# Kernel tuning notes

Measured on AMD Instinct MI355X. Metric: run time of the kernel, lower is better.

## Reference

```python
import jax, jax.numpy as jnp
import numpy as np

NINP, NHID, NOUT = 400, 600, 400
HS = NHID + NOUT          # h_size = nhid + nout
NLEVELS, K, AUX_FREQ = 40, 2, 20
DILATION = [1]


def setup_inputs() -> dict:
    key = jax.random.key(0)
    ks = jax.random.split(key, 6)
    B, T = 8, 256
    bound = 0.01  # matches init_weights normal_(0, 0.01)
    return {
        "X": jax.random.normal(ks[0], (B, NINP, T), jnp.float32),
        "hid": jax.random.normal(ks[1], (B, HS, 1), jnp.float32),
        "cell": jax.random.normal(ks[2], (B, HS, 1), jnp.float32),
        "w1": jax.random.normal(ks[3], (4 * HS, NINP, K), jnp.float32) * bound,
        "w2": jax.random.normal(ks[4], (4 * HS, HS, K), jnp.float32) * bound,
        "b2": jax.random.normal(ks[5], (4 * HS,), jnp.float32) * bound,
    }


def _conv1d(x, w, d):
    # x: [B, Cin, T_padded], w: [Cout, Cin, K] -> [B, Cout, T]
    return jax.lax.conv_general_dilated(
        x, w, window_strides=(1,), padding='VALID', rhs_dilation=(d,),
        dimension_numbers=('NCH', 'OIH', 'NCH'))


def _forward(X, hid, cell, w1, w2, b2):
    B, _, T = X.shape
    ht = jnp.zeros((B, HS, T), X.dtype)
    ct = jnp.zeros((B, HS, T), X.dtype)

    # Input-side convolution is weight-tied and X never changes across levels,
    # so (like the torch dict cache) compute it once per distinct dilation.
    conv1 = {}
    for d in set(DILATION):
        pad = (K - 1) * d
        xp = jnp.pad(X, ((0, 0), (0, 0), (pad, 0)))
        conv1[d] = _conv1d(xp, w1, d)

    aux = []
    for i in range(NLEVELS):
        d = DILATION[i % len(DILATION)]
        pad = (K - 1) * d
        # causal left-pad of the hidden stream, filled with the initial hid
        z1 = jnp.concatenate([jnp.broadcast_to(hid, (B, HS, pad)), ht], axis=2)
        out = conv1[d] + _conv1d(z1, w2, d) + b2[None, :, None]  # [B, 4*HS, T]
        # shifted cell state, first d steps filled with the initial cell
        ct_1 = jnp.concatenate(
            [jnp.broadcast_to(cell, (B, HS, d)), ct[:, :, :-d]], axis=2)
        it = jax.nn.sigmoid(out[:, :HS])
        ot = jax.nn.sigmoid(out[:, HS:2 * HS])
        gt = jnp.tanh(out[:, 2 * HS:3 * HS])
        ft = jax.nn.sigmoid(out[:, 3 * HS:])
        ct = ft * ct_1 + it * gt
        ht = ot * jnp.tanh(ct)
        if i % AUX_FREQ == AUX_FREQ - 1:
            aux.append(ht[:, -NOUT:])  # [B, nout, T]

    out_main = jnp.transpose(ht[:, -NOUT:], (0, 2, 1))            # [B, T, nout]
    hc = (ht[:, :, -1:], ct[:, :, -1:])                            # ([B,HS,1], [B,HS,1])
    aux_outs = jnp.transpose(jnp.stack(aux, axis=0), (1, 0, 3, 2))  # [B, n_aux, T, nout]
    return out_main, hc, aux_outs


def reference(X, hid, cell, w1, w2, b2):
    return _forward(X, hid, cell, w1, w2, b2)
```

## Files before the change

kernel.cpp:

```cpp
#include <hip/hip_runtime.h>
#include <hip/hip_bf16.h>
#include <math.h>

typedef __bf16 bf16;
typedef __bf16 bf16x8 __attribute__((ext_vector_type(8)));
typedef __bf16 bf16x4 __attribute__((ext_vector_type(4)));
typedef float f32x4 __attribute__((ext_vector_type(4)));
typedef float f32x16 __attribute__((ext_vector_type(16)));
typedef unsigned int u32;
typedef u32 u32x4 __attribute__((ext_vector_type(4)));

#define NINP 400
#define HS   1000
#define HP   1024
#define B_   8
#define T_   256
#define NT   2048
#define K2   2048
#define K1   1024
#define M_   4096

#define HT_OFF   819200
#define CT_OFF   827200
#define AUX_OFF  835200

__device__ __forceinline__ float sigm(float x) { return 1.0f / (1.0f + expf(-x)); }


__global__ void repack_w1(const float* __restrict__ w1, bf16* __restrict__ W1q) {
  int idx = blockIdx.x * 256 + threadIdx.x;
  if (idx >= M_ * K1) return;
  int m = idx >> 10, k = idx & 1023;
  int g = (m >> 3) & 3, h = (m >> 5) * 8 + (m & 7);
  float v = 0.0f;
  if (h < HS) {
    int c = g * HS + h;
    if (k < 512) { if (k < NINP) v = w1[(size_t)c * (NINP * 2) + k * 2 + 0]; }
    else { int j = k - 512; if (j < NINP) v = w1[(size_t)c * (NINP * 2) + j * 2 + 1]; }
  }
  W1q[idx] = (bf16)v;
}

__global__ void repack_w2(const float* __restrict__ w2, bf16* __restrict__ W2q) {
  int idx = blockIdx.x * 256 + threadIdx.x;
  if (idx >= M_ * K2) return;
  int m = idx >> 11, k = idx & 2047;
  int g = (m >> 3) & 3, h = (m >> 5) * 8 + (m & 7);
  float v = 0.0f;
  if (h < HS) {
    int c = g * HS + h;
    if (k < HP) { if (k < HS) v = w2[(size_t)c * (HS * 2) + k * 2 + 0]; }
    else { int j = k - HP; if (j < HS) v = w2[(size_t)c * (HS * 2) + j * 2 + 1]; }
  }
  W2q[idx] = (bf16)v;
}

__global__ void build_xt(const float* __restrict__ X, bf16* __restrict__ XT) {
  int idx = blockIdx.x * 256 + threadIdx.x;
  if (idx >= NT * K1) return;
  int n = idx >> 10, k = idx & 1023;
  int b = n >> 8, t = n & (T_ - 1);
  float v = 0.0f;
  if (k < 512) { if (k < NINP && t > 0) v = X[((size_t)b * NINP + k) * T_ + t - 1]; }
  else { int j = k - 512; if (j < NINP) v = X[((size_t)b * NINP + j) * T_ + t]; }
  XT[idx] = (bf16)v;
}

__global__ void build_hc(const float* __restrict__ hid, const float* __restrict__ cell,
                         bf16* __restrict__ hidp, float* __restrict__ cellp) {
  int idx = blockIdx.x * 256 + threadIdx.x;
  if (idx >= B_ * HP) return;
  int b = idx >> 10, k = idx & (HP - 1);
  hidp[idx]  = (k < HS) ? (bf16)hid[b * HS + k] : (bf16)0.0f;
  cellp[idx] = (k < HS) ? cell[b * HS + k] : 0.0f;
}


template <bool GATED>
__global__ __launch_bounds__(256, 2) void gemm_step(
    const bf16* __restrict__ A,
    const bf16* __restrict__ Bsrc,
    const bf16* __restrict__ hidp,
    const bf16* __restrict__ CbIn,
    bf16* __restrict__ CbOut,
    const float* __restrict__ b2,
    const bf16* __restrict__ ctprev,
    const float* __restrict__ cellp,
    bf16* __restrict__ ctnew,
    bf16* __restrict__ Hnew,
    int K) {
  __shared__ bf16 As[2][128][64];
  __shared__ bf16 Bs[2][128][64];

  const int tid = threadIdx.x;
  const int lane = tid & 63;
  const int w = tid >> 6;
  const int mh = w >> 1, nh = w & 1;
  const int c8 = tid & 7;
  const int sr = tid >> 3;
  const int row32 = lane & 31;
  const int q2 = lane >> 5;
  const int physw = ((c8 + sr) & 7) * 8;

  int n0, bm;
  if (GATED) {
    const int L = blockIdx.y * gridDim.x + blockIdx.x;
    bm = (L & 7) * 4 + (L >> 7);
    n0 = ((L >> 3) & 15) * 128;
  } else {
    n0 = blockIdx.x * 128;
    bm = blockIdx.y;
  }

  const int NIT = K >> 6;
  const bf16* Abase = A + (size_t)(bm * 128 + sr) * K + c8 * 8;

  auto loadA = [&](int site, int k0) -> u32x4 {
    return *(const u32x4*)(Abase + (size_t)site * 32 * K + k0);
  };
  auto loadB = [&](int site, int k0) -> u32x4 {
    const int n = n0 + site * 32 + sr;
    const bf16* bp;
    if (GATED) {
      if (k0 < HP) {
        const int t = n & (T_ - 1);
        bp = (t == 0) ? (hidp + (size_t)(n >> 8) * HP + k0)
                      : (Bsrc + (size_t)(n - 1) * HP + k0);
      } else {
        bp = Bsrc + (size_t)n * HP + (k0 - HP);
      }
    } else {
      bp = Bsrc + (size_t)n * K + k0;
    }
    return *(const u32x4*)(bp + c8 * 8);
  };

  f32x16 acc[2][2];
#pragma unroll
  for (int i = 0; i < 2; ++i)
#pragma unroll
    for (int j = 0; j < 2; ++j)
#pragma unroll
      for (int e = 0; e < 16; ++e) acc[i][j][e] = 0.0f;

  u32x4 ra[4], rb[4];
#pragma unroll
  for (int s = 0; s < 4; ++s) { ra[s] = loadA(s, 0); rb[s] = loadB(s, 0); }
#pragma unroll
  for (int s = 0; s < 4; ++s) {
    *(u32x4*)&As[0][s * 32 + sr][physw] = ra[s];
    *(u32x4*)&Bs[0][s * 32 + sr][physw] = rb[s];
  }

  for (int it = 0; it < NIT; ++it) {
    const int p = it & 1;
    if (it + 1 < NIT) {
      const int k0 = (it + 1) << 6;
#pragma unroll
      for (int s = 0; s < 4; ++s) { ra[s] = loadA(s, k0); rb[s] = loadB(s, k0); }
    }
    __syncthreads();
#pragma unroll
    for (int kc = 0; kc < 4; ++kc) {
      const int l = kc * 2 + q2;
      bf16x8 av[2], bv[2];
#pragma unroll
      for (int mt = 0; mt < 2; ++mt) {
        const int r = mh * 64 + mt * 32 + row32;
        av[mt] = *(const bf16x8*)&As[p][r][((l + r) & 7) * 8];
      }
#pragma unroll
      for (int nt = 0; nt < 2; ++nt) {
        const int r = nh * 64 + nt * 32 + row32;
        bv[nt] = *(const bf16x8*)&Bs[p][r][((l + r) & 7) * 8];
      }
#pragma unroll
      for (int mt = 0; mt < 2; ++mt)
#pragma unroll
        for (int nt = 0; nt < 2; ++nt)
          acc[mt][nt] = __builtin_amdgcn_mfma_f32_32x32x16_bf16(av[mt], bv[nt], acc[mt][nt], 0, 0, 0);
    }
    if (it + 1 < NIT) {
      const int q = p ^ 1;
#pragma unroll
      for (int s = 0; s < 4; ++s) {
        *(u32x4*)&As[q][s * 32 + sr][physw] = ra[s];
        *(u32x4*)&Bs[q][s * 32 + sr][physw] = rb[s];
      }
    }
  }

  if (!GATED) {
    __syncthreads();
    bf16 (*Csh)[128] = (bf16(*)[128])&As[0][0][0];
#pragma unroll
    for (int mt = 0; mt < 2; ++mt) {
      const int tt = mh * 2 + mt;
#pragma unroll
      for (int nt = 0; nt < 2; ++nt) {
        const int nloc = nh * 64 + nt * 32 + row32;
#pragma unroll
        for (int g = 0; g < 4; ++g) {
          bf16x4 v;
#pragma unroll
          for (int j = 0; j < 4; ++j) {
            const int h = bm * 32 + tt * 8 + 4 * q2 + j;
            const float bias = (h < HS) ? b2[g * HS + h] : 0.0f;
            v[j] = (bf16)(acc[mt][nt][g * 4 + j] + bias);
          }
          *(bf16x4*)&Csh[nloc][tt * 32 + g * 8 + 4 * q2] = v;
        }
      }
    }
    __syncthreads();
#pragma unroll
    for (int i2 = 0; i2 < 8; ++i2) {
      const int idx = i2 * 256 + tid;
      const int rrow = idx >> 4, off = idx & 15;
      *(u32x4*)&CbOut[(size_t)(n0 + rrow) * 4096 + bm * 128 + off * 8] =
          *(const u32x4*)&Csh[rrow][off * 8];
    }
  } else {
    bf16 (*Hsh)[32] = (bf16(*)[32])&As[0][0][0];
#pragma unroll
    for (int mt = 0; mt < 2; ++mt) {
      const int tt = mh * 2 + mt;
#pragma unroll
      for (int nt = 0; nt < 2; ++nt) {
        const int nloc = nh * 64 + nt * 32 + row32;
        const int n = n0 + nloc;
        const int b = n >> 8;
        const int t = n & (T_ - 1);
        const size_t cb = (size_t)n * 4096 + (size_t)(bm * 4 + tt) * 32 + 4 * q2;
        bf16x4 c0 = *(const bf16x4*)&CbIn[cb + 0];
        bf16x4 c1 = *(const bf16x4*)&CbIn[cb + 8];
        bf16x4 c2 = *(const bf16x4*)&CbIn[cb + 16];
        bf16x4 c3 = *(const bf16x4*)&CbIn[cb + 24];
        bf16x4 hv;
#pragma unroll
        for (int j = 0; j < 4; ++j) {
          const int h = bm * 32 + tt * 8 + 4 * q2 + j;
          const float ci = acc[mt][nt][0 + j]  + (float)c0[j];
          const float co = acc[mt][nt][4 + j]  + (float)c1[j];
          const float cg = acc[mt][nt][8 + j]  + (float)c2[j];
          const float cf = acc[mt][nt][12 + j] + (float)c3[j];
          const float ctold = (t == 0) ? cellp[b * HP + h]
                                       : (float)ctprev[(size_t)h * NT + (n - 1)];
          const float cn = sigm(cf) * ctold + sigm(ci) * tanhf(cg);
          ctnew[(size_t)h * NT + n] = (bf16)cn;
          hv[j] = (bf16)(sigm(co) * tanhf(cn));
        }
        *(bf16x4*)&Hsh[nloc][tt * 8 + 4 * q2] = hv;
      }
    }
    __syncthreads();
#pragma unroll
    for (int i2 = 0; i2 < 2; ++i2) {
      const int idx = i2 * 256 + tid;
      const int rrow = idx >> 2, off = idx & 3;
      *(u32x4*)&Hnew[(size_t)(n0 + rrow) * HP + bm * 32 + off * 8] =
          *(const u32x4*)&Hsh[rrow][off * 8];
    }
  }
}


__global__ void aux_kernel(const bf16* __restrict__ H, float* __restrict__ out, int s) {
  int idx = blockIdx.x * 256 + threadIdx.x;
  if (idx >= NT * 100) return;
  int n = idx / 100;
  int o = (idx % 100) * 4;
  int b = n >> 8, t = n & (T_ - 1);
  bf16x4 v = *(const bf16x4*)&H[(size_t)n * HP + 600 + o];
  f32x4 f = {(float)v[0], (float)v[1], (float)v[2], (float)v[3]};
  *(f32x4*)&out[AUX_OFF + ((size_t)((b * 2 + s) * T_ + t)) * 400 + o] = f;
}

__global__ void final_kernel(const bf16* __restrict__ H, const bf16* __restrict__ ct,
                             float* __restrict__ out) {
  int idx = blockIdx.x * 256 + threadIdx.x;
  if (idx < NT * 100) {
    int n = idx / 100;
    int o = (idx % 100) * 4;
    int b = n >> 8, t = n & (T_ - 1);
    bf16x4 v = *(const bf16x4*)&H[(size_t)n * HP + 600 + o];
    f32x4 f = {(float)v[0], (float)v[1], (float)v[2], (float)v[3]};
    *(f32x4*)&out[(size_t)n * 400 + o] = f;
    *(f32x4*)&out[AUX_OFF + ((size_t)((b * 2 + 1) * T_ + t)) * 400 + o] = f;
  } else {
    int j = idx - NT * 100;
    if (j < 8000) {
      int b = j / 1000, h = j % 1000;
      out[HT_OFF + j] = (float)H[(size_t)(b * T_ + 255) * HP + h];
    } else if (j < 16000) {
      int jj = j - 8000;
      int b = jj / 1000, h = jj % 1000;
      out[CT_OFF + jj] = (float)ct[(size_t)h * NT + b * T_ + 255];
    }
  }
}


extern "C" void kernel_launch(void* const* d_in, const int* in_sizes, int n_in,
                              void* d_out, int out_size, void* d_ws, size_t ws_size,
                              hipStream_t stream) {
  const float* X    = (const float*)d_in[0];
  const float* hid  = (const float*)d_in[1];
  const float* cell = (const float*)d_in[2];
  const float* w1   = (const float*)d_in[3];
  const float* w2   = (const float*)d_in[4];
  const float* b2   = (const float*)d_in[5];
  float* out = (float*)d_out;

  char* ws = (char*)d_ws;
  size_t off = 0;
  auto alloc = [&](size_t bytes) {
    void* p = ws + off;
    off += (bytes + 255) & ~(size_t)255;
    return p;
  };
  bf16* W2q    = (bf16*)alloc((size_t)M_ * K2 * 2);
  bf16* CbP    = (bf16*)alloc((size_t)NT * M_ * 2);
  bf16* Hb0    = (bf16*)alloc((size_t)NT * HP * 2);
  bf16* ctb0   = (bf16*)alloc((size_t)HP * NT * 2);
  bf16* hidp   = (bf16*)alloc((size_t)B_ * HP * 2);
  float* cellp = (float*)alloc((size_t)B_ * HP * 4);
  char* R = (char*)alloc((size_t)12 * 1024 * 1024);
  bf16* W1q  = (bf16*)R;
  bf16* XT   = (bf16*)(R + (size_t)8 * 1024 * 1024);
  bf16* ctb1 = (bf16*)R;
  bf16* Hb1  = (bf16*)(R + (size_t)4 * 1024 * 1024);

  bf16* Hb[2]  = {Hb0, Hb1};
  bf16* ctb[2] = {ctb0, ctb1};

  hipMemsetAsync(Hb[0], 0, (size_t)NT * HP * 2, stream);
  hipMemsetAsync(ctb[0], 0, (size_t)HP * NT * 2, stream);

  repack_w1<<<(M_ * K1) / 256, 256, 0, stream>>>(w1, W1q);
  repack_w2<<<(M_ * K2) / 256, 256, 0, stream>>>(w2, W2q);
  build_xt<<<(NT * K1) / 256, 256, 0, stream>>>(X, XT);
  build_hc<<<(B_ * HP) / 256, 256, 0, stream>>>(hid, cell, hidp, cellp);

  dim3 grid(NT / 128, M_ / 128);
  gemm_step<false><<<grid, 256, 0, stream>>>(W1q, XT, nullptr, nullptr, CbP, b2,
                                             nullptr, nullptr, nullptr, nullptr, K1);
  for (int i = 0; i < 40; ++i) {
    int p = i & 1;
    gemm_step<true><<<grid, 256, 0, stream>>>(W2q, Hb[p], hidp, CbP, nullptr, nullptr,
                                              ctb[p], cellp, ctb[p ^ 1], Hb[p ^ 1], K2);
    if (i == 19) aux_kernel<<<800, 256, 0, stream>>>(Hb[p ^ 1], out, 0);
  }
  final_kernel<<<(NT * 100 + 16000 + 255) / 256, 256, 0, stream>>>(Hb[0], ctb[0], out);
}
```

Before: 2.140 ms.

## Pre-swizzle weights into MFMA fragment order and load B via async global-to-LDS

Weights are repacked into the per-lane MFMA fragment layout, so each wave reads its A operands straight from global memory into registers without staging them in LDS. The B tile is copied into LDS with global_load_lds async copies, using a swizzled source offset to avoid bank conflicts. The old register-staged double buffer is dropped: there is now a single LDS buffer with two barriers per k-step, and the LDS footprint is smaller. This is meant to cut LDS traffic and VGPR pressure, but it loses the explicit prefetch overlap, and A now depends on global and cache latency.

```diff
diff --git a/kernel.cpp b/kernel.cpp
--- a/kernel.cpp
+++ b/kernel.cpp
@@ -24,35 +24,46 @@
 #define CT_OFF   827200
 #define AUX_OFF  835200
 
+typedef __attribute__((address_space(1))) const void gvoid;
+typedef __attribute__((address_space(3))) void lvoid;
+
+__device__ __forceinline__ void async_copy16(void* lds, const void* g) {
+  __builtin_amdgcn_global_load_lds((gvoid*)g, (lvoid*)lds, 16, 0, 0);
+}
+
 __device__ __forceinline__ float sigm(float x) { return 1.0f / (1.0f + expf(-x)); }
 
 
-__global__ void repack_w1(const float* __restrict__ w1, bf16* __restrict__ W1q) {
+__global__ void repack_w2(const float* __restrict__ w2, bf16* __restrict__ W2f) {
+  int idx = blockIdx.x * 256 + threadIdx.x;
+  if (idx >= M_ * K2) return;
+  int j = idx & 7, lane = (idx >> 3) & 63, kt = (idx >> 9) & 127, mtile = idx >> 16;
+  int m = mtile * 32 + (lane & 31);
+  int k = kt * 16 + (lane >> 5) * 8 + j;
+  int g = (m >> 3) & 3, h = (m >> 5) * 8 + (m & 7);
+  float v = 0.0f;
+  if (h < HS) {
+    int c = g * HS + h;
+    if (k < HP) { if (k < HS) v = w2[(size_t)c * (HS * 2) + k * 2 + 0]; }
+    else { int kk = k - HP; if (kk < HS) v = w2[(size_t)c * (HS * 2) + kk * 2 + 1]; }
+  }
+  W2f[idx] = (bf16)v;
+}
+
+__global__ void repack_w1(const float* __restrict__ w1, bf16* __restrict__ W1f) {
   int idx = blockIdx.x * 256 + threadIdx.x;
   if (idx >= M_ * K1) return;
-  int m = idx >> 10, k = idx & 1023;
+  int j = idx & 7, lane = (idx >> 3) & 63, kt = (idx >> 9) & 63, mtile = idx >> 15;
+  int m = mtile * 32 + (lane & 31);
+  int k = kt * 16 + (lane >> 5) * 8 + j;
   int g = (m >> 3) & 3, h = (m >> 5) * 8 + (m & 7);
   float v = 0.0f;
   if (h < HS) {
     int c = g * HS + h;
     if (k < 512) { if (k < NINP) v = w1[(size_t)c * (NINP * 2) + k * 2 + 0]; }
-    else { int j = k - 512; if (j < NINP) v = w1[(size_t)c * (NINP * 2) + j * 2 + 1]; }
-  }
-  W1q[idx] = (bf16)v;
-}
-
-__global__ void repack_w2(const float* __restrict__ w2, bf16* __restrict__ W2q) {
-  int idx = blockIdx.x * 256 + threadIdx.x;
-  if (idx >= M_ * K2) return;
-  int m = idx >> 11, k = idx & 2047;
-  int g = (m >> 3) & 3, h = (m >> 5) * 8 + (m & 7);
-  float v = 0.0f;
-  if (h < HS) {
-    int c = g * HS + h;
-    if (k < HP) { if (k < HS) v = w2[(size_t)c * (HS * 2) + k * 2 + 0]; }
-    else { int j = k - HP; if (j < HS) v = w2[(size_t)c * (HS * 2) + j * 2 + 1]; }
-  }
-  W2q[idx] = (bf16)v;
+    else { int kk = k - 512; if (kk < NINP) v = w1[(size_t)c * (NINP * 2) + kk * 2 + 1]; }
+  }
+  W1f[idx] = (bf16)v;
 }
 
 __global__ void build_xt(const float* __restrict__ X, bf16* __restrict__ XT) {
@@ -78,7 +89,7 @@
 
 template <bool GATED>
 __global__ __launch_bounds__(256, 2) void gemm_step(
-    const bf16* __restrict__ A,
+    const bf16* __restrict__ Af,
     const bf16* __restrict__ Bsrc,
     const bf16* __restrict__ hidp,
     const bf16* __restrict__ CbIn,
@@ -89,18 +100,16 @@
     bf16* __restrict__ ctnew,
     bf16* __restrict__ Hnew,
     int K) {
-  __shared__ bf16 As[2][128][64];
-  __shared__ bf16 Bs[2][128][64];
+  __shared__ bf16 SMEM[128 * 128];
+  bf16 (*Bs)[64] = (bf16(*)[64])SMEM;
 
   const int tid = threadIdx.x;
   const int lane = tid & 63;
   const int w = tid >> 6;
   const int mh = w >> 1, nh = w & 1;
-  const int c8 = tid & 7;
-  const int sr = tid >> 3;
-  const int row32 = lane & 31;
-  const int q2 = lane >> 5;
-  const int physw = ((c8 + sr) & 7) * 8;
+  const int dr = lane >> 3, c8 = lane & 7;
+  const int swo = ((c8 - dr) & 7) * 8;
+  const int row32 = lane & 31, q2 = lane >> 5;
 
   int n0, bm;
   if (GATED) {
@@ -112,87 +121,68 @@
     bm = blockIdx.y;
   }
 
+  const int NKT = K >> 4;
+  const bf16* A0 = Af + ((size_t)(bm * 4 + mh * 2 + 0) * NKT * 64 + lane) * 8;
+  const bf16* A1 = Af + ((size_t)(bm * 4 + mh * 2 + 1) * NKT * 64 + lane) * 8;
+
+  f32x16 acc[2][2];
+#pragma unroll
+  for (int i = 0; i < 2; ++i)
+#pragma unroll
+    for (int j = 0; j < 2; ++j)
+#pragma unroll
+      for (int e = 0; e < 16; ++e) acc[i][j][e] = 0.0f;
+
   const int NIT = K >> 6;
-  const bf16* Abase = A + (size_t)(bm * 128 + sr) * K + c8 * 8;
-
-  auto loadA = [&](int site, int k0) -> u32x4 {
-    return *(const u32x4*)(Abase + (size_t)site * 32 * K + k0);
-  };
-  auto loadB = [&](int site, int k0) -> u32x4 {
-    const int n = n0 + site * 32 + sr;
-    const bf16* bp;
-    if (GATED) {
-      if (k0 < HP) {
-        const int t = n & (T_ - 1);
-        bp = (t == 0) ? (hidp + (size_t)(n >> 8) * HP + k0)
-                      : (Bsrc + (size_t)(n - 1) * HP + k0);
+  for (int it = 0; it < NIT; ++it) {
+    const int k0 = it << 6;
+    __syncthreads();
+#pragma unroll
+    for (int inst = 0; inst < 4; ++inst) {
+      const int r = inst * 32 + w * 8 + dr;
+      const int n = n0 + r;
+      const bf16* bp;
+      if (GATED) {
+        const int kk = (k0 & (HP - 1)) + swo;
+        if (k0 < HP) {
+          const int t = n & (T_ - 1);
+          bp = (t == 0) ? (hidp + (size_t)(n >> 8) * HP + kk)
+                        : (Bsrc + (size_t)(n - 1) * HP + kk);
+        } else {
+          bp = Bsrc + (size_t)n * HP + kk;
+        }
       } else {
-        bp = Bsrc + (size_t)n * HP + (k0 - HP);
+        bp = Bsrc + (size_t)n * K + k0 + swo;
       }
-    } else {
-      bp = Bsrc + (size_t)n * K + k0;
-    }
-    return *(const u32x4*)(bp + c8 * 8);
-  };
-
-  f32x16 acc[2][2];
-#pragma unroll
-  for (int i = 0; i < 2; ++i)
-#pragma unroll
-    for (int j = 0; j < 2; ++j)
-#pragma unroll
-      for (int e = 0; e < 16; ++e) acc[i][j][e] = 0.0f;
-
-  u32x4 ra[4], rb[4];
-#pragma unroll
-  for (int s = 0; s < 4; ++s) { ra[s] = loadA(s, 0); rb[s] = loadB(s, 0); }
-#pragma unroll
-  for (int s = 0; s < 4; ++s) {
-    *(u32x4*)&As[0][s * 32 + sr][physw] = ra[s];
-    *(u32x4*)&Bs[0][s * 32 + sr][physw] = rb[s];
-  }
-
-  for (int it = 0; it < NIT; ++it) {
-    const int p = it & 1;
-    if (it + 1 < NIT) {
-      const int k0 = (it + 1) << 6;
-#pragma unroll
-      for (int s = 0; s < 4; ++s) { ra[s] = loadA(s, k0); rb[s] = loadB(s, k0); }
+      async_copy16(&Bs[inst * 32 + w * 8][0], bp);
+    }
+    bf16x8 af[2][4];
+#pragma unroll
+    for (int kc = 0; kc < 4; ++kc) {
+      af[0][kc] = *(const bf16x8*)(A0 + (size_t)(it * 4 + kc) * 512);
+      af[1][kc] = *(const bf16x8*)(A1 + (size_t)(it * 4 + kc) * 512);
     }
     __syncthreads();
 #pragma unroll
     for (int kc = 0; kc < 4; ++kc) {
       const int l = kc * 2 + q2;
-      bf16x8 av[2], bv[2];
-#pragma unroll
-      for (int mt = 0; mt < 2; ++mt) {
-        const int r = mh * 64 + mt * 32 + row32;
-        av[mt] = *(const bf16x8*)&As[p][r][((l + r) & 7) * 8];
-      }
+      bf16x8 bv[2];
 #pragma unroll
       for (int nt = 0; nt < 2; ++nt) {
         const int r = nh * 64 + nt * 32 + row32;
-        bv[nt] = *(const bf16x8*)&Bs[p][r][((l + r) & 7) * 8];
+        bv[nt] = *(const bf16x8*)&Bs[r][((l + r) & 7) * 8];
       }
 #pragma unroll
       for (int mt = 0; mt < 2; ++mt)
 #pragma unroll
         for (int nt = 0; nt < 2; ++nt)
-          acc[mt][nt] = __builtin_amdgcn_mfma_f32_32x32x16_bf16(av[mt], bv[nt], acc[mt][nt], 0, 0, 0);
-    }
-    if (it + 1 < NIT) {
-      const int q = p ^ 1;
-#pragma unroll
-      for (int s = 0; s < 4; ++s) {
-        *(u32x4*)&As[q][s * 32 + sr][physw] = ra[s];
-        *(u32x4*)&Bs[q][s * 32 + sr][physw] = rb[s];
-      }
+          acc[mt][nt] = __builtin_amdgcn_mfma_f32_32x32x16_bf16(af[mt][kc], bv[nt], acc[mt][nt], 0, 0, 0);
     }
   }
 
   if (!GATED) {
     __syncthreads();
-    bf16 (*Csh)[128] = (bf16(*)[128])&As[0][0][0];
+    bf16 (*Csh)[128] = (bf16(*)[128])SMEM;
 #pragma unroll
     for (int mt = 0; mt < 2; ++mt) {
       const int tt = mh * 2 + mt;
@@ -221,7 +211,8 @@
           *(const u32x4*)&Csh[rrow][off * 8];
     }
   } else {
-    bf16 (*Hsh)[32] = (bf16(*)[32])&As[0][0][0];
+    __syncthreads();
+    bf16 (*Hsh)[32] = (bf16(*)[32])SMEM;
 #pragma unroll
     for (int mt = 0; mt < 2; ++mt) {
       const int tt = mh * 2 + mt;
@@ -319,14 +310,14 @@
     off += (bytes + 255) & ~(size_t)255;
     return p;
   };
-  bf16* W2q    = (bf16*)alloc((size_t)M_ * K2 * 2);
+  bf16* W2f    = (bf16*)alloc((size_t)M_ * K2 * 2);
   bf16* CbP    = (bf16*)alloc((size_t)NT * M_ * 2);
   bf16* Hb0    = (bf16*)alloc((size_t)NT * HP * 2);
   bf16* ctb0   = (bf16*)alloc((size_t)HP * NT * 2);
   bf16* hidp   = (bf16*)alloc((size_t)B_ * HP * 2);
   float* cellp = (float*)alloc((size_t)B_ * HP * 4);
   char* R = (char*)alloc((size_t)12 * 1024 * 1024);
-  bf16* W1q  = (bf16*)R;
+  bf16* W1f  = (bf16*)R;
   bf16* XT   = (bf16*)(R + (size_t)8 * 1024 * 1024);
   bf16* ctb1 = (bf16*)R;
   bf16* Hb1  = (bf16*)(R + (size_t)4 * 1024 * 1024);
@@ -337,17 +328,17 @@
   hipMemsetAsync(Hb[0], 0, (size_t)NT * HP * 2, stream);
   hipMemsetAsync(ctb[0], 0, (size_t)HP * NT * 2, stream);
 
-  repack_w1<<<(M_ * K1) / 256, 256, 0, stream>>>(w1, W1q);
-  repack_w2<<<(M_ * K2) / 256, 256, 0, stream>>>(w2, W2q);
+  repack_w1<<<(M_ * K1) / 256, 256, 0, stream>>>(w1, W1f);
+  repack_w2<<<(M_ * K2) / 256, 256, 0, stream>>>(w2, W2f);
   build_xt<<<(NT * K1) / 256, 256, 0, stream>>>(X, XT);
   build_hc<<<(B_ * HP) / 256, 256, 0, stream>>>(hid, cell, hidp, cellp);
 
   dim3 grid(NT / 128, M_ / 128);
-  gemm_step<false><<<grid, 256, 0, stream>>>(W1q, XT, nullptr, nullptr, CbP, b2,
+  gemm_step<false><<<grid, 256, 0, stream>>>(W1f, XT, nullptr, nullptr, CbP, b2,
                                              nullptr, nullptr, nullptr, nullptr, K1);
   for (int i = 0; i < 40; ++i) {
     int p = i & 1;
-    gemm_step<true><<<grid, 256, 0, stream>>>(W2q, Hb[p], hidp, CbP, nullptr, nullptr,
+    gemm_step<true><<<grid, 256, 0, stream>>>(W2f, Hb[p], hidp, CbP, nullptr, nullptr,
                                               ctb[p], cellp, ctb[p ^ 1], Hb[p ^ 1], K2);
     if (i == 19) aux_kernel<<<800, 256, 0, stream>>>(Hb[p ^ 1], out, 0);
   }
```

New measurement: 2.151 ms. No clear change (+0.5%).

## Stage GEMM tiles via direct global-to-LDS async loads, prefetch CbIn early

Applied to the files above, without the earlier changes.

Replaces the register-staged, double-buffered LDS pipeline with direct global_load_lds copies into a single LDS buffer per operand, moving the swizzle onto the source address. The gated epilogue's CbIn reads are issued before the K loop so their latency overlaps the GEMM. This drops VGPR staging and LDS store instructions and halves LDS use, which may raise occupancy. The cost is losing overlap between the next tile's loads and the current MFMAs, since each iteration now waits on its own loads behind a barrier.

```diff
diff --git a/kernel.cpp b/kernel.cpp
--- a/kernel.cpp
+++ b/kernel.cpp
@@ -23,6 +23,13 @@
 #define HT_OFF   819200
 #define CT_OFF   827200
 #define AUX_OFF  835200
+
+typedef __attribute__((address_space(1))) const void gvoid;
+typedef __attribute__((address_space(3))) void lvoid;
+
+__device__ __forceinline__ void async_copy16(void* lds, const void* g) {
+  __builtin_amdgcn_global_load_lds((gvoid*)g, (lvoid*)lds, 16, 0, 0);
+}
 
 __device__ __forceinline__ float sigm(float x) { return 1.0f / (1.0f + expf(-x)); }
 
@@ -89,18 +96,15 @@
     bf16* __restrict__ ctnew,
     bf16* __restrict__ Hnew,
     int K) {
-  __shared__ bf16 As[2][128][64];
-  __shared__ bf16 Bs[2][128][64];
+  __shared__ bf16 SMEM[2][128][64];
 
   const int tid = threadIdx.x;
   const int lane = tid & 63;
   const int w = tid >> 6;
   const int mh = w >> 1, nh = w & 1;
-  const int c8 = tid & 7;
-  const int sr = tid >> 3;
-  const int row32 = lane & 31;
-  const int q2 = lane >> 5;
-  const int physw = ((c8 + sr) & 7) * 8;
+  const int dr = lane >> 3, c8 = lane & 7;
+  const int swo = ((c8 - dr) & 7) * 8;
+  const int row32 = lane & 31, q2 = lane >> 5;
 
   int n0, bm;
   if (GATED) {
@@ -112,52 +116,54 @@
     bm = blockIdx.y;
   }
 
+  f32x16 acc[2][2];
+#pragma unroll
+  for (int i = 0; i < 2; ++i)
+#pragma unroll
+    for (int j = 0; j < 2; ++j)
+#pragma unroll
+      for (int e = 0; e < 16; ++e) acc[i][j][e] = 0.0f;
+
+  bf16x4 cbr[2][2][4];
+  if (GATED) {
+#pragma unroll
+    for (int mt = 0; mt < 2; ++mt) {
+      const int tt = mh * 2 + mt;
+#pragma unroll
+      for (int nt = 0; nt < 2; ++nt) {
+        const int n = n0 + nh * 64 + nt * 32 + row32;
+        const size_t cb = (size_t)n * 4096 + (size_t)(bm * 4 + tt) * 32 + 4 * q2;
+#pragma unroll
+        for (int g = 0; g < 4; ++g)
+          cbr[mt][nt][g] = *(const bf16x4*)&CbIn[cb + g * 8];
+      }
+    }
+  }
+
   const int NIT = K >> 6;
-  const bf16* Abase = A + (size_t)(bm * 128 + sr) * K + c8 * 8;
-
-  auto loadA = [&](int site, int k0) -> u32x4 {
-    return *(const u32x4*)(Abase + (size_t)site * 32 * K + k0);
-  };
-  auto loadB = [&](int site, int k0) -> u32x4 {
-    const int n = n0 + site * 32 + sr;
-    const bf16* bp;
-    if (GATED) {
-      if (k0 < HP) {
-        const int t = n & (T_ - 1);
-        bp = (t == 0) ? (hidp + (size_t)(n >> 8) * HP + k0)
-                      : (Bsrc + (size_t)(n - 1) * HP + k0);
+  for (int it = 0; it < NIT; ++it) {
+    const int k0 = it << 6;
+    __syncthreads();
+#pragma unroll
+    for (int inst = 0; inst < 4; ++inst) {
+      const int r = inst * 32 + w * 8 + dr;
+      async_copy16(&SMEM[0][inst * 32 + w * 8][0],
+                   A + (size_t)(bm * 128 + r) * K + k0 + swo);
+      const int n = n0 + r;
+      const bf16* bp;
+      if (GATED) {
+        const int kk = (k0 & (HP - 1)) + swo;
+        if (k0 < HP) {
+          const int t = n & (T_ - 1);
+          bp = (t == 0) ? (hidp + (size_t)(n >> 8) * HP + kk)
+                        : (Bsrc + (size_t)(n - 1) * HP + kk);
+        } else {
+          bp = Bsrc + (size_t)n * HP + kk;
+        }
       } else {
-        bp = Bsrc + (size_t)n * HP + (k0 - HP);
-      }
-    } else {
-      bp = Bsrc + (size_t)n * K + k0;
-    }
-    return *(const u32x4*)(bp + c8 * 8);
-  };
-
-  f32x16 acc[2][2];
-#pragma unroll
-  for (int i = 0; i < 2; ++i)
-#pragma unroll
-    for (int j = 0; j < 2; ++j)
-#pragma unroll
-      for (int e = 0; e < 16; ++e) acc[i][j][e] = 0.0f;
-
-  u32x4 ra[4], rb[4];
-#pragma unroll
-  for (int s = 0; s < 4; ++s) { ra[s] = loadA(s, 0); rb[s] = loadB(s, 0); }
-#pragma unroll
-  for (int s = 0; s < 4; ++s) {
-    *(u32x4*)&As[0][s * 32 + sr][physw] = ra[s];
-    *(u32x4*)&Bs[0][s * 32 + sr][physw] = rb[s];
-  }
-
-  for (int it = 0; it < NIT; ++it) {
-    const int p = it & 1;
-    if (it + 1 < NIT) {
-      const int k0 = (it + 1) << 6;
-#pragma unroll
-      for (int s = 0; s < 4; ++s) { ra[s] = loadA(s, k0); rb[s] = loadB(s, k0); }
+        bp = Bsrc + (size_t)n * K + k0 + swo;
+      }
+      async_copy16(&SMEM[1][inst * 32 + w * 8][0], bp);
     }
     __syncthreads();
 #pragma unroll
@@ -167,12 +173,12 @@
 #pragma unroll
       for (int mt = 0; mt < 2; ++mt) {
         const int r = mh * 64 + mt * 32 + row32;
-        av[mt] = *(const bf16x8*)&As[p][r][((l + r) & 7) * 8];
+        av[mt] = *(const bf16x8*)&SMEM[0][r][((l + r) & 7) * 8];
       }
 #pragma unroll
       for (int nt = 0; nt < 2; ++nt) {
         const int r = nh * 64 + nt * 32 + row32;
-        bv[nt] = *(const bf16x8*)&Bs[p][r][((l + r) & 7) * 8];
+        bv[nt] = *(const bf16x8*)&SMEM[1][r][((l + r) & 7) * 8];
       }
 #pragma unroll
       for (int mt = 0; mt < 2; ++mt)
@@ -180,19 +186,11 @@
         for (int nt = 0; nt < 2; ++nt)
           acc[mt][nt] = __builtin_amdgcn_mfma_f32_32x32x16_bf16(av[mt], bv[nt], acc[mt][nt], 0, 0, 0);
     }
-    if (it + 1 < NIT) {
-      const int q = p ^ 1;
-#pragma unroll
-      for (int s = 0; s < 4; ++s) {
-        *(u32x4*)&As[q][s * 32 + sr][physw] = ra[s];
-        *(u32x4*)&Bs[q][s * 32 + sr][physw] = rb[s];
-      }
-    }
   }
 
   if (!GATED) {
     __syncthreads();
-    bf16 (*Csh)[128] = (bf16(*)[128])&As[0][0][0];
+    bf16 (*Csh)[128] = (bf16(*)[128])&SMEM[0][0][0];
 #pragma unroll
     for (int mt = 0; mt < 2; ++mt) {
       const int tt = mh * 2 + mt;
@@ -221,7 +219,8 @@
           *(const u32x4*)&Csh[rrow][off * 8];
     }
   } else {
-    bf16 (*Hsh)[32] = (bf16(*)[32])&As[0][0][0];
+    __syncthreads();
+    bf16 (*Hsh)[32] = (bf16(*)[32])&SMEM[0][0][0];
 #pragma unroll
     for (int mt = 0; mt < 2; ++mt) {
       const int tt = mh * 2 + mt;
@@ -231,19 +230,14 @@
         const int n = n0 + nloc;
         const int b = n >> 8;
         const int t = n & (T_ - 1);
-        const size_t cb = (size_t)n * 4096 + (size_t)(bm * 4 + tt) * 32 + 4 * q2;
-        bf16x4 c0 = *(const bf16x4*)&CbIn[cb + 0];
-        bf16x4 c1 = *(const bf16x4*)&CbIn[cb + 8];
-        bf16x4 c2 = *(const bf16x4*)&CbIn[cb + 16];
-        bf16x4 c3 = *(const bf16x4*)&CbIn[cb + 24];
         bf16x4 hv;
 #pragma unroll
         for (int j = 0; j < 4; ++j) {
           const int h = bm * 32 + tt * 8 + 4 * q2 + j;
-          const float ci = acc[mt][nt][0 + j]  + (float)c0[j];
-          const float co = acc[mt][nt][4 + j]  + (float)c1[j];
-          const float cg = acc[mt][nt][8 + j]  + (float)c2[j];
-          const float cf = acc[mt][nt][12 + j] + (float)c3[j];
+          const float ci = acc[mt][nt][0 + j]  + (float)cbr[mt][nt][0][j];
+          const float co = acc[mt][nt][4 + j]  + (float)cbr[mt][nt][1][j];
+          const float cg = acc[mt][nt][8 + j]  + (float)cbr[mt][nt][2][j];
+          const float cf = acc[mt][nt][12 + j] + (float)cbr[mt][nt][3][j];
           const float ctold = (t == 0) ? cellp[b * HP + h]
                                        : (float)ctprev[(size_t)h * NT + (n - 1)];
           const float cn = sigm(cf) * ctold + sigm(ci) * tanhf(cg);
```

After: 2.423 ms. +13.2%, slower.
